# Optimization experiments

Hardware: AMD Instinct MI355X
Metric: run time of the kernel (lower is better)

The kernel has to match this reference:

```python
import jax, jax.numpy as jnp
import numpy as np

DIM = 1024
HEADS = 16
DIM_HEAD = 64
INNER = HEADS * DIM_HEAD
EPS = 1e-5


def setup_inputs() -> dict:
    key = jax.random.key(0)
    ks = jax.random.split(key, 6)
    x = jax.random.normal(ks[0], (2, 2048, DIM), dtype=jnp.float32)
    gamma = jax.random.normal(ks[1], (DIM,), dtype=jnp.float32) * 0.02 + 1.0
    beta = jax.random.normal(ks[2], (DIM,), dtype=jnp.float32) * 0.02
    # weights stored [in, out] (transpose of torch Linear convention)
    w_qkv = jax.random.normal(ks[3], (DIM, INNER * 3), dtype=jnp.float32) / np.sqrt(DIM)
    w_out = jax.random.normal(ks[4], (INNER, DIM), dtype=jnp.float32) / np.sqrt(INNER)
    b_out = jax.random.normal(ks[5], (DIM,), dtype=jnp.float32) * 0.02
    return {"x": x, "gamma": gamma, "beta": beta, "w_qkv": w_qkv, "w_out": w_out, "b_out": b_out}


def _attention(x, gamma, beta, w_qkv, w_out, b_out):
    b, n, d = x.shape
    # layernorm over last dim (biased variance), then affine
    mu = jnp.mean(x, axis=-1, keepdims=True)
    var = jnp.mean(jnp.square(x - mu), axis=-1, keepdims=True)
    xn = (x - mu) * jax.lax.rsqrt(var + EPS) * gamma + beta
    qkv = xn @ w_qkv  # [b, n, 3*inner]
    q, k, v = jnp.split(qkv, 3, axis=-1)
    split_heads = lambda t: t.reshape(b, n, HEADS, DIM_HEAD).transpose(0, 2, 1, 3)  # [b,h,n,dh]
    q, k, v = map(split_heads, (q, k, v))
    q = q * (DIM_HEAD ** -0.5)
    sim = jnp.einsum('bhid,bhjd->bhij', q, k)  # full [b,h,n,n] as in the original
    attn = jax.nn.softmax(sim, axis=-1)
    out = jnp.einsum('bhij,bhjd->bhid', attn, v)
    out = out.transpose(0, 2, 1, 3).reshape(b, n, INNER)
    return out @ w_out + b_out


def reference(x, gamma, beta, w_qkv, w_out, b_out):
    return _attention(x, gamma, beta, w_qkv, w_out, b_out)
```

## Files before the change

### kernel.cpp

```cpp
#include <hip/hip_runtime.h>

typedef unsigned short u16;
typedef __attribute__((ext_vector_type(8))) __bf16 bf16x8;
typedef __attribute__((ext_vector_type(4))) float f32x4;

#define GLD_LDS(src, dst) \
  __builtin_amdgcn_global_load_lds((const __attribute__((address_space(1))) void*)(src), \
                                   (__attribute__((address_space(3))) void*)(dst), 16, 0, 0)

__device__ __forceinline__ u16 f2bf(float f) {
  union { float f; unsigned int u; } c; c.f = f;
  unsigned int u = c.u + 0x7FFFu + ((c.u >> 16) & 1u);
  return (u16)(u >> 16);
}

__device__ __forceinline__ unsigned int cvt_pk_bf16(float lo, float hi) {
  unsigned int r;
  asm("v_cvt_pk_bf16_f32 %0, %1, %2" : "=v"(r) : "v"(lo), "v"(hi));
  return r;
}

__global__ __launch_bounds__(256) void ln_kernel(const float* __restrict__ x,
    const float* __restrict__ gamma, const float* __restrict__ beta,
    u16* __restrict__ xn)
{
  const int row = blockIdx.x, tid = threadIdx.x;
  const int lane = tid & 63, wave = tid >> 6;
  const float4 v = ((const float4*)(x + (size_t)row * 1024))[tid];
  float s = v.x + v.y + v.z + v.w;
  float q = v.x*v.x + v.y*v.y + v.z*v.z + v.w*v.w;
  #pragma unroll
  for (int m = 1; m < 64; m <<= 1) { s += __shfl_xor(s, m, 64); q += __shfl_xor(q, m, 64); }
  __shared__ float red[8];
  if (lane == 0) { red[wave] = s; red[4 + wave] = q; }
  __syncthreads();
  s = red[0] + red[1] + red[2] + red[3];
  q = red[4] + red[5] + red[6] + red[7];
  const float mu = s * (1.0f/1024.0f);
  const float var = q * (1.0f/1024.0f) - mu*mu;
  const float rs = rsqrtf(var + 1e-5f);
  const float4 gm = ((const float4*)gamma)[tid];
  const float4 bt = ((const float4*)beta)[tid];
  unsigned int w0 = (unsigned int)f2bf((v.x - mu)*rs*gm.x + bt.x)
                  | ((unsigned int)f2bf((v.y - mu)*rs*gm.y + bt.y) << 16);
  unsigned int w1 = (unsigned int)f2bf((v.z - mu)*rs*gm.z + bt.z)
                  | ((unsigned int)f2bf((v.w - mu)*rs*gm.w + bt.w) << 16);
  uint2 o; o.x = w0; o.y = w1;
  ((uint2*)(xn + (size_t)row * 1024))[tid] = o;
}

__global__ void transpose_cvt(const float* __restrict__ in, u16* __restrict__ out,
                              int K, int N, int scaleLim)
{
  __shared__ float t[32][33];
  const int n0 = blockIdx.x * 32, k0 = blockIdx.y * 32;
  const int lx = threadIdx.x, ly = threadIdx.y;
  #pragma unroll
  for (int i = 0; i < 32; i += 8)
    t[ly + i][lx] = in[(size_t)(k0 + ly + i) * N + n0 + lx];
  __syncthreads();
  #pragma unroll
  for (int i = 0; i < 32; i += 8) {
    int n = n0 + ly + i;
    float v = t[lx][ly + i];
    if (n < scaleLim) v *= 0.18033688011116011f;
    out[(size_t)n * K + k0 + lx] = f2bf(v);
  }
}

__device__ __forceinline__ int vpos(int n) {
  return (n & ~63) | (n & 0x23) | ((n & 0x0C) << 1) | ((n & 0x10) >> 2);
}

__global__ __launch_bounds__(256) void vt_kernel(const u16* __restrict__ qkv,
                                                 u16* __restrict__ vt)
{
  const int bh = blockIdx.y, b = bh >> 4, h = bh & 15;
  const int d = threadIdx.x & 63, n8 = threadIdx.x >> 6;
  const int n = blockIdx.x * 32 + n8 * 8;
  const u16* src = qkv + (size_t)(b * 2048 + n) * 3072 + 2048 + h * 64 + d;
  unsigned int w[4];
  #pragma unroll
  for (int p = 0; p < 4; ++p) {
    unsigned int lo = src[(size_t)(2*p) * 3072];
    unsigned int hi = src[(size_t)(2*p + 1) * 3072];
    w[p] = lo | (hi << 16);
  }
  u16* dst = vt + ((size_t)bh * 64 + d) * 2048;
  uint2 o0; o0.x = w[0]; o0.y = w[1];
  uint2 o1; o1.x = w[2]; o1.y = w[3];
  *(uint2*)&dst[vpos(n)] = o0;
  *(uint2*)&dst[vpos(n + 4)] = o1;
}

template<bool FINAL, int BN>
__global__ __launch_bounds__(256, 2) void gemm_bt(
    const u16* __restrict__ A, const u16* __restrict__ BT,
    u16* __restrict__ outB, float* __restrict__ outF,
    const float* __restrict__ bias, int M, int N, int K)
{
  constexpr int NF = BN / 32;
  __shared__ __align__(16) u16 Alds[128 * 64];
  __shared__ __align__(16) u16 Blds[BN * 64];
  const int tid = threadIdx.x, wave = tid >> 6, lane = tid & 63;
  const int r15 = lane & 15, g = lane >> 4, l8 = lane >> 3, c8 = lane & 7;

  const int nwgx = gridDim.x;
  const int lin = blockIdx.x + blockIdx.y * nwgx;
  const int cpx = (nwgx * gridDim.y) >> 3;
  const int swz = (lin & 7) * cpx + (lin >> 3);
  const int row0 = (swz / nwgx) * 128, col0 = (swz % nwgx) * BN;

  const int wm = (wave >> 1) * 64, wn = (wave & 1) * (BN / 2);
  const int srcCol = (c8 ^ l8) << 3;

  f32x4 acc[4][NF] = {};

  for (int kt = 0; kt < K; kt += 64) {
    #pragma unroll
    for (int c = 0; c < 4; ++c) {
      const int r0 = wave * 32 + c * 8;
      GLD_LDS(A + (size_t)(row0 + r0 + l8) * K + kt + srcCol, Alds + r0 * 64);
    }
    #pragma unroll
    for (int c = 0; c < NF; ++c) {
      const int r0 = wave * (BN / 4) + c * 8;
      GLD_LDS(BT + (size_t)(col0 + r0 + l8) * K + kt + srcCol, Blds + r0 * 64);
    }
    __syncthreads();
    #pragma unroll
    for (int kk = 0; kk < 2; ++kk) {
      bf16x8 af[4], bf[NF];
      #pragma unroll
      for (int m = 0; m < 4; ++m) {
        const int row = wm + m * 16 + r15;
        af[m] = *(const bf16x8*)((const char*)Alds + row * 128 + ((kk*64 + g*16) ^ ((row & 7) << 4)));
      }
      #pragma unroll
      for (int n = 0; n < NF; ++n) {
        const int row = wn + n * 16 + r15;
        bf[n] = *(const bf16x8*)((const char*)Blds + row * 128 + ((kk*64 + g*16) ^ ((row & 7) << 4)));
      }
      #pragma unroll
      for (int m = 0; m < 4; ++m)
        #pragma unroll
        for (int n = 0; n < NF; ++n)
          acc[m][n] = __builtin_amdgcn_mfma_f32_16x16x32_bf16(af[m], bf[n], acc[m][n], 0, 0, 0);
    }
    __syncthreads();
  }

  #pragma unroll
  for (int m = 0; m < 4; ++m)
    #pragma unroll
    for (int n = 0; n < NF; ++n) {
      const int row = row0 + wm + m * 16 + g * 4;
      const int col = col0 + wn + n * 16 + r15;
      if constexpr (FINAL) {
        const float bv = bias[col];
        #pragma unroll
        for (int r = 0; r < 4; ++r)
          outF[(size_t)(row + r) * N + col] = acc[m][n][r] + bv;
      } else {
        #pragma unroll
        for (int r = 0; r < 4; ++r)
          outB[(size_t)(row + r) * N + col] = f2bf(acc[m][n][r]);
      }
    }
}

__global__ __launch_bounds__(256, 4) void attn_kernel(const u16* __restrict__ qkv,
                                                      const u16* __restrict__ vt,
                                                      u16* __restrict__ attnO)
{
  __shared__ __align__(16) u16 Klds[2][64 * 64];
  __shared__ __align__(16) u16 Vlds[2][64 * 64];

  const int tid = threadIdx.x, wave = tid >> 6, lane = tid & 63;
  const int r15 = lane & 15, g = lane >> 4, l8 = lane >> 3, c8 = lane & 7;
  const int bh = blockIdx.x, qt = blockIdx.y;
  const int b = bh >> 4, h = bh & 15;

  const u16* Qp = qkv + (size_t)b * 2048 * 3072 + h * 64;
  const u16* Kp = Qp + 1024;
  const u16* Vt = vt + (size_t)bh * 64 * 2048;

  const int q0 = qt * 64 + wave * 16;

  bf16x8 qf[2];
  #pragma unroll
  for (int kk = 0; kk < 2; ++kk)
    qf[kk] = *(const bf16x8*)(Qp + (size_t)(q0 + r15) * 3072 + kk*32 + g*8);

  f32x4 acc[4] = {};
  f32x4 accl = {};

  const int srcCol = (c8 ^ l8) << 3;

  const unsigned int one2 = 0x3F803F80u;
  uint4 onesu; onesu.x = one2; onesu.y = one2; onesu.z = one2; onesu.w = one2;
  const bf16x8 onesf = *(const bf16x8*)&onesu;

  int offp[2][4];
  #pragma unroll
  for (int kk = 0; kk < 2; ++kk)
    #pragma unroll
    for (int m = 0; m < 4; ++m)
      offp[kk][m] = (m * 16 + r15) * 128 + ((kk * 64 + g * 16) ^ ((r15 & 7) << 4));

  #pragma unroll
  for (int c = 0; c < 2; ++c) {
    const int r0 = wave * 16 + c * 8;
    GLD_LDS(Kp + (size_t)(r0 + l8) * 3072 + srcCol, &Klds[0][r0 * 64]);
    GLD_LDS(Vt + (size_t)(r0 + l8) * 2048 + srcCol, &Vlds[0][r0 * 64]);
  }
  __syncthreads();

  #pragma unroll 2
  for (int kt = 0; kt < 32; ++kt) {
    const int cur = kt & 1;
    if (kt < 31) {
      const int nxt = cur ^ 1, kn = kt + 1;
      #pragma unroll
      for (int c = 0; c < 2; ++c) {
        const int r0 = wave * 16 + c * 8;
        GLD_LDS(Kp + (size_t)(kn*64 + r0 + l8) * 3072 + srcCol, &Klds[nxt][r0 * 64]);
        GLD_LDS(Vt + (size_t)(r0 + l8) * 2048 + kn*64 + srcCol, &Vlds[nxt][r0 * 64]);
      }
    }

    const char* kbase = (const char*)&Klds[cur][0];
    bf16x8 kf[2][4];
    #pragma unroll
    for (int kk = 0; kk < 2; ++kk)
      #pragma unroll
      for (int m = 0; m < 4; ++m)
        kf[kk][m] = *(const bf16x8*)(kbase + offp[kk][m]);
    f32x4 s[4] = {};
    #pragma unroll
    for (int kk = 0; kk < 2; ++kk)
      #pragma unroll
      for (int m = 0; m < 4; ++m)
        s[m] = __builtin_amdgcn_mfma_f32_16x16x32_bf16(kf[kk][m], qf[kk], s[m], 0, 0, 0);

    #pragma unroll
    for (int m = 0; m < 4; ++m)
      #pragma unroll
      for (int r = 0; r < 4; ++r)
        s[m][r] = __builtin_amdgcn_exp2f(s[m][r]);

    unsigned int u[4][2];
    #pragma unroll
    for (int m = 0; m < 4; ++m) {
      u[m][0] = cvt_pk_bf16(s[m][0], s[m][1]);
      u[m][1] = cvt_pk_bf16(s[m][2], s[m][3]);
    }
    uint4 pw[2];
    pw[0].x = u[0][0]; pw[0].y = u[0][1]; pw[0].z = u[1][0]; pw[0].w = u[1][1];
    pw[1].x = u[2][0]; pw[1].y = u[2][1]; pw[1].z = u[3][0]; pw[1].w = u[3][1];

    const char* vbase = (const char*)&Vlds[cur][0];
    bf16x8 vf[2][4];
    #pragma unroll
    for (int kk = 0; kk < 2; ++kk)
      #pragma unroll
      for (int nf = 0; nf < 4; ++nf)
        vf[kk][nf] = *(const bf16x8*)(vbase + offp[kk][nf]);
    #pragma unroll
    for (int kk = 0; kk < 2; ++kk) {
      const bf16x8 pfk = *(const bf16x8*)&pw[kk];
      accl = __builtin_amdgcn_mfma_f32_16x16x32_bf16(onesf, pfk, accl, 0, 0, 0);
      #pragma unroll
      for (int nf = 0; nf < 4; ++nf)
        acc[nf] = __builtin_amdgcn_mfma_f32_16x16x32_bf16(vf[kk][nf], pfk, acc[nf], 0, 0, 0);
    }

    __syncthreads();
  }

  const float linv = 1.0f / accl[0];
  const size_t base = (size_t)(b * 2048 + q0 + r15) * 1024 + h * 64;
  #pragma unroll
  for (int nf = 0; nf < 4; ++nf) {
    uint2 o;
    o.x = cvt_pk_bf16(acc[nf][0] * linv, acc[nf][1] * linv);
    o.y = cvt_pk_bf16(acc[nf][2] * linv, acc[nf][3] * linv);
    *(uint2*)&attnO[base + nf*16 + g*4] = o;
  }
}

extern "C" void kernel_launch(void* const* d_in, const int* in_sizes, int n_in,
                              void* d_out, int out_size, void* d_ws, size_t ws_size,
                              hipStream_t stream) {
  const float* x     = (const float*)d_in[0];
  const float* gamma = (const float*)d_in[1];
  const float* beta  = (const float*)d_in[2];
  const float* w_qkv = (const float*)d_in[3];
  const float* w_out = (const float*)d_in[4];
  const float* b_out = (const float*)d_in[5];
  float* out = (float*)d_out;
  char* ws = (char*)d_ws;

  u16* xn    = (u16*)(ws);
  u16* vtbuf = (u16*)(ws);
  u16* wqkvT = (u16*)(ws + ( 8u << 20));
  u16* qkv   = (u16*)(ws + (14u << 20));
  u16* woutT = (u16*)(ws + (38u << 20));
  u16* attnO = (u16*)(ws + (40u << 20));

  ln_kernel<<<4096, 256, 0, stream>>>(x, gamma, beta, xn);
  transpose_cvt<<<dim3(96, 32), dim3(32, 8), 0, stream>>>(w_qkv, wqkvT, 1024, 3072, 1024);
  transpose_cvt<<<dim3(32, 32), dim3(32, 8), 0, stream>>>(w_out, woutT, 1024, 1024, 0);
  gemm_bt<false, 128><<<dim3(24, 32), 256, 0, stream>>>(xn, wqkvT, qkv, nullptr, nullptr, 4096, 3072, 1024);
  vt_kernel<<<dim3(64, 32), 256, 0, stream>>>(qkv, vtbuf);
  attn_kernel<<<dim3(32, 32), 256, 0, stream>>>(qkv, vtbuf, attnO);
  gemm_bt<true, 64><<<dim3(16, 32), 256, 0, stream>>>(attnO, woutT, nullptr, out, b_out, 4096, 1024, 1024);
}
```

Baseline: 116.6 us.

## Fuse V transpose into QKV GEMM epilogue and drop vt_kernel

The QKV GEMM epilogue now writes Q and K into a compact 2048-wide buffer and writes V directly into the transposed, permuted per-head layout that the attention kernel expects. This removes the separate vt_kernel launch and its extra read and write of V. The GEMM is templated on the wave grid, but it is still launched with a 2x2 grid. The attention kernel strides are updated for the narrower Q/K buffer. The V epilogue stores are 8-byte scattered writes across rows of the transposed buffer, which may coalesce less well than the row-major stores.

```diff
diff --git a/kernel.cpp b/kernel.cpp
--- a/kernel.cpp
+++ b/kernel.cpp
@@ -18,6 +18,10 @@
   unsigned int r;
   asm("v_cvt_pk_bf16_f32 %0, %1, %2" : "=v"(r) : "v"(lo), "v"(hi));
   return r;
+}
+
+__device__ __forceinline__ int vpos(int n) {
+  return (n & ~63) | (n & 0x23) | ((n & 0x0C) << 1) | ((n & 0x10) >> 2);
 }
 
 __global__ __launch_bounds__(256) void ln_kernel(const float* __restrict__ x,
@@ -68,38 +72,15 @@
   }
 }
 
-__device__ __forceinline__ int vpos(int n) {
-  return (n & ~63) | (n & 0x23) | ((n & 0x0C) << 1) | ((n & 0x10) >> 2);
-}
-
-__global__ __launch_bounds__(256) void vt_kernel(const u16* __restrict__ qkv,
-                                                 u16* __restrict__ vt)
-{
-  const int bh = blockIdx.y, b = bh >> 4, h = bh & 15;
-  const int d = threadIdx.x & 63, n8 = threadIdx.x >> 6;
-  const int n = blockIdx.x * 32 + n8 * 8;
-  const u16* src = qkv + (size_t)(b * 2048 + n) * 3072 + 2048 + h * 64 + d;
-  unsigned int w[4];
-  #pragma unroll
-  for (int p = 0; p < 4; ++p) {
-    unsigned int lo = src[(size_t)(2*p) * 3072];
-    unsigned int hi = src[(size_t)(2*p + 1) * 3072];
-    w[p] = lo | (hi << 16);
-  }
-  u16* dst = vt + ((size_t)bh * 64 + d) * 2048;
-  uint2 o0; o0.x = w[0]; o0.y = w[1];
-  uint2 o1; o1.x = w[2]; o1.y = w[3];
-  *(uint2*)&dst[vpos(n)] = o0;
-  *(uint2*)&dst[vpos(n + 4)] = o1;
-}
-
-template<bool FINAL, int BN>
-__global__ __launch_bounds__(256, 2) void gemm_bt(
+template<bool FINAL, int BN, int WM, int WN>
+__global__ __launch_bounds__(WM*WN*64, 2) void gemm_bt(
     const u16* __restrict__ A, const u16* __restrict__ BT,
-    u16* __restrict__ outB, float* __restrict__ outF,
+    u16* __restrict__ outB, u16* __restrict__ outV, float* __restrict__ outF,
     const float* __restrict__ bias, int M, int N, int K)
 {
-  constexpr int NF = BN / 32;
+  constexpr int TW = WM * WN;
+  constexpr int MF = 128 / (16 * WM);
+  constexpr int NF = BN / (16 * WN);
   __shared__ __align__(16) u16 Alds[128 * 64];
   __shared__ __align__(16) u16 Blds[BN * 64];
   const int tid = threadIdx.x, wave = tid >> 6, lane = tid & 63;
@@ -111,28 +92,29 @@
   const int swz = (lin & 7) * cpx + (lin >> 3);
   const int row0 = (swz / nwgx) * 128, col0 = (swz % nwgx) * BN;
 
-  const int wm = (wave >> 1) * 64, wn = (wave & 1) * (BN / 2);
+  const int wm = (wave / WN) * (128 / WM);
+  const int wn = (wave % WN) * (BN / WN);
   const int srcCol = (c8 ^ l8) << 3;
 
-  f32x4 acc[4][NF] = {};
+  f32x4 acc[MF][NF] = {};
 
   for (int kt = 0; kt < K; kt += 64) {
     #pragma unroll
-    for (int c = 0; c < 4; ++c) {
-      const int r0 = wave * 32 + c * 8;
+    for (int c = 0; c < 16 / TW; ++c) {
+      const int r0 = wave * (128 / TW) + c * 8;
       GLD_LDS(A + (size_t)(row0 + r0 + l8) * K + kt + srcCol, Alds + r0 * 64);
     }
     #pragma unroll
-    for (int c = 0; c < NF; ++c) {
-      const int r0 = wave * (BN / 4) + c * 8;
+    for (int c = 0; c < BN / (8 * TW); ++c) {
+      const int r0 = wave * (BN / TW) + c * 8;
       GLD_LDS(BT + (size_t)(col0 + r0 + l8) * K + kt + srcCol, Blds + r0 * 64);
     }
     __syncthreads();
     #pragma unroll
     for (int kk = 0; kk < 2; ++kk) {
-      bf16x8 af[4], bf[NF];
-      #pragma unroll
-      for (int m = 0; m < 4; ++m) {
+      bf16x8 af[MF], bf[NF];
+      #pragma unroll
+      for (int m = 0; m < MF; ++m) {
         const int row = wm + m * 16 + r15;
         af[m] = *(const bf16x8*)((const char*)Alds + row * 128 + ((kk*64 + g*16) ^ ((row & 7) << 4)));
       }
@@ -142,7 +124,7 @@
         bf[n] = *(const bf16x8*)((const char*)Blds + row * 128 + ((kk*64 + g*16) ^ ((row & 7) << 4)));
       }
       #pragma unroll
-      for (int m = 0; m < 4; ++m)
+      for (int m = 0; m < MF; ++m)
         #pragma unroll
         for (int n = 0; n < NF; ++n)
           acc[m][n] = __builtin_amdgcn_mfma_f32_16x16x32_bf16(af[m], bf[n], acc[m][n], 0, 0, 0);
@@ -150,26 +132,49 @@
     __syncthreads();
   }
 
-  #pragma unroll
-  for (int m = 0; m < 4; ++m)
-    #pragma unroll
-    for (int n = 0; n < NF; ++n) {
-      const int row = row0 + wm + m * 16 + g * 4;
-      const int col = col0 + wn + n * 16 + r15;
-      if constexpr (FINAL) {
+  if constexpr (FINAL) {
+    #pragma unroll
+    for (int m = 0; m < MF; ++m)
+      #pragma unroll
+      for (int n = 0; n < NF; ++n) {
+        const int row = row0 + wm + m * 16 + g * 4;
+        const int col = col0 + wn + n * 16 + r15;
         const float bv = bias[col];
         #pragma unroll
         for (int r = 0; r < 4; ++r)
           outF[(size_t)(row + r) * N + col] = acc[m][n][r] + bv;
-      } else {
+      }
+  } else {
+    if (col0 < 2048) {
+      #pragma unroll
+      for (int m = 0; m < MF; ++m)
         #pragma unroll
-        for (int r = 0; r < 4; ++r)
-          outB[(size_t)(row + r) * N + col] = f2bf(acc[m][n][r]);
-      }
-    }
-}
-
-__global__ __launch_bounds__(256, 4) void attn_kernel(const u16* __restrict__ qkv,
+        for (int n = 0; n < NF; ++n) {
+          const int row = row0 + wm + m * 16 + g * 4;
+          const int col = col0 + wn + n * 16 + r15;
+          #pragma unroll
+          for (int r = 0; r < 4; ++r)
+            outB[(size_t)(row + r) * 2048 + col] = f2bf(acc[m][n][r]);
+        }
+    } else {
+      #pragma unroll
+      for (int m = 0; m < MF; ++m)
+        #pragma unroll
+        for (int n = 0; n < NF; ++n) {
+          const int row = row0 + wm + m * 16 + g * 4;
+          const int bb = row >> 11, ns = row & 2047;
+          const int hh = (col0 + wn - 2048) >> 6;
+          const int dd = (wn + n * 16 + r15) & 63;
+          uint2 o;
+          o.x = cvt_pk_bf16(acc[m][n][0], acc[m][n][1]);
+          o.y = cvt_pk_bf16(acc[m][n][2], acc[m][n][3]);
+          *(uint2*)&outV[((size_t)((bb * 16 + hh) * 64 + dd)) * 2048 + vpos(ns)] = o;
+        }
+    }
+  }
+}
+
+__global__ __launch_bounds__(256, 4) void attn_kernel(const u16* __restrict__ qkvQK,
                                                       const u16* __restrict__ vt,
                                                       u16* __restrict__ attnO)
 {
@@ -181,7 +186,7 @@
   const int bh = blockIdx.x, qt = blockIdx.y;
   const int b = bh >> 4, h = bh & 15;
 
-  const u16* Qp = qkv + (size_t)b * 2048 * 3072 + h * 64;
+  const u16* Qp = qkvQK + (size_t)b * 2048 * 2048 + h * 64;
   const u16* Kp = Qp + 1024;
   const u16* Vt = vt + (size_t)bh * 64 * 2048;
 
@@ -190,7 +195,7 @@
   bf16x8 qf[2];
   #pragma unroll
   for (int kk = 0; kk < 2; ++kk)
-    qf[kk] = *(const bf16x8*)(Qp + (size_t)(q0 + r15) * 3072 + kk*32 + g*8);
+    qf[kk] = *(const bf16x8*)(Qp + (size_t)(q0 + r15) * 2048 + kk*32 + g*8);
 
   f32x4 acc[4] = {};
   f32x4 accl = {};
@@ -211,7 +216,7 @@
   #pragma unroll
   for (int c = 0; c < 2; ++c) {
     const int r0 = wave * 16 + c * 8;
-    GLD_LDS(Kp + (size_t)(r0 + l8) * 3072 + srcCol, &Klds[0][r0 * 64]);
+    GLD_LDS(Kp + (size_t)(r0 + l8) * 2048 + srcCol, &Klds[0][r0 * 64]);
     GLD_LDS(Vt + (size_t)(r0 + l8) * 2048 + srcCol, &Vlds[0][r0 * 64]);
   }
   __syncthreads();
@@ -224,7 +229,7 @@
       #pragma unroll
       for (int c = 0; c < 2; ++c) {
         const int r0 = wave * 16 + c * 8;
-        GLD_LDS(Kp + (size_t)(kn*64 + r0 + l8) * 3072 + srcCol, &Klds[nxt][r0 * 64]);
+        GLD_LDS(Kp + (size_t)(kn*64 + r0 + l8) * 2048 + srcCol, &Klds[nxt][r0 * 64]);
         GLD_LDS(Vt + (size_t)(r0 + l8) * 2048 + kn*64 + srcCol, &Vlds[nxt][r0 * 64]);
       }
     }
@@ -302,17 +307,16 @@
   char* ws = (char*)d_ws;
 
   u16* xn    = (u16*)(ws);
-  u16* vtbuf = (u16*)(ws);
   u16* wqkvT = (u16*)(ws + ( 8u << 20));
-  u16* qkv   = (u16*)(ws + (14u << 20));
+  u16* qkvQK = (u16*)(ws + (14u << 20));
+  u16* vtbuf = (u16*)(ws + (30u << 20));
   u16* woutT = (u16*)(ws + (38u << 20));
   u16* attnO = (u16*)(ws + (40u << 20));
 
   ln_kernel<<<4096, 256, 0, stream>>>(x, gamma, beta, xn);
   transpose_cvt<<<dim3(96, 32), dim3(32, 8), 0, stream>>>(w_qkv, wqkvT, 1024, 3072, 1024);
   transpose_cvt<<<dim3(32, 32), dim3(32, 8), 0, stream>>>(w_out, woutT, 1024, 1024, 0);
-  gemm_bt<false, 128><<<dim3(24, 32), 256, 0, stream>>>(xn, wqkvT, qkv, nullptr, nullptr, 4096, 3072, 1024);
-  vt_kernel<<<dim3(64, 32), 256, 0, stream>>>(qkv, vtbuf);
-  attn_kernel<<<dim3(32, 32), 256, 0, stream>>>(qkv, vtbuf, attnO);
-  gemm_bt<true, 64><<<dim3(16, 32), 256, 0, stream>>>(attnO, woutT, nullptr, out, b_out, 4096, 1024, 1024);
-}
+  gemm_bt<false, 128, 2, 2><<<dim3(24, 32), 256, 0, stream>>>(xn, wqkvT, qkvQK, vtbuf, nullptr, nullptr, 4096, 3072, 1024);
+  attn_kernel<<<dim3(32, 32), 256, 0, stream>>>(qkvQK, vtbuf, attnO);
+  gemm_bt<true, 64, 2, 2><<<dim3(16, 32), 256, 0, stream>>>(attnO, woutT, nullptr, nullptr, out, b_out, 4096, 1024, 1024);
+}
```

Result: faster. 106.8 us (-8.4%).
